# Kernel tuning notes

Hardware: AMD Instinct MI355X
Metric: run time of the kernel (lower is better)

The kernel has to match this reference:

```python
import jax, jax.numpy as jnp
import numpy as np
import math

FACTOR = 1

def setup_inputs() -> dict:
    key = jax.random.key(0)
    k1, k2, k3 = jax.random.split(key, 3)
    B, L, H, E = 32, 1024, 8, 64
    return {
        "queries": jax.random.normal(k1, (B, L, H, E), dtype=jnp.float32),
        "keys": jax.random.normal(k2, (B, L, H, E), dtype=jnp.float32),
        "values": jax.random.normal(k3, (B, L, H, E), dtype=jnp.float32),
        "attn_mask": 0,
    }


def reference(queries, keys, values, attn_mask):
    # queries/keys/values: [B, L, H, E] (S == L so no pad/truncate needed)
    B, L, H, E = queries.shape
    q = jnp.transpose(queries, (0, 2, 3, 1))  # [B,H,E,L]
    k = jnp.transpose(keys, (0, 2, 3, 1))
    v = jnp.transpose(values, (0, 2, 3, 1))   # [B,H,D,L]

    # FFT cross-correlation
    q_fft = jnp.fft.rfft(q, axis=-1)
    k_fft = jnp.fft.rfft(k, axis=-1)
    corr = jnp.fft.irfft(q_fft * jnp.conj(k_fft), n=L, axis=-1)  # [B,H,E,L]

    # top-k delay selection (global over batch, as in source)
    top_k = min(int(FACTOR * math.log(L)), L // 4, 32)  # static: 6
    mean_value = corr.mean(axis=(1, 2))                 # [B,L]
    weights, indices = jax.lax.top_k(mean_value.mean(axis=0), top_k)  # [k]
    tmp_corr = jax.nn.softmax(weights)                  # [k]

    # weighted circular-shift aggregation: roll(v, -indices[i]) summed with tmp_corr[i]
    pos = (jnp.arange(L)[None, :] + indices[:, None]) % L  # [k,L]
    patterns = v[:, :, :, pos]                              # [B,H,D,k,L]
    delays_agg = jnp.einsum('k,bhdkl->bhdl', tmp_corr, patterns)

    return jnp.transpose(delays_agg, (0, 3, 1, 2))  # [B,L,H,D]
```

## Files before the change

kernel.cpp:

```cpp
#include <hip/hip_runtime.h>
#include <math.h>

#define L_SEQ 1024
#define HE 512
#define NBATCH 32
#define TOPK 6
#define NZ 32

using bf16x8 = __attribute__((ext_vector_type(8))) short;
using f32x4  = __attribute__((ext_vector_type(4))) float;
using f32x2v = __attribute__((ext_vector_type(2))) float;
using bfx2v  = __attribute__((ext_vector_type(2))) __bf16;

__device__ __forceinline__ unsigned int bf2(float lo, float hi) {
  f32x2v f; f[0] = lo; f[1] = hi;
  bfx2v h = __builtin_convertvector(f, bfx2v);
  return *(unsigned int*)&h;
}

__global__ __launch_bounds__(512, 2) void gram_fused_kernel(
    const float* __restrict__ q, const float* __restrict__ k,
    float* __restrict__ partial)
{
  __shared__ char smem[71680];
  char* As = smem;
  char* Bs = smem + 32768;

  const int tid = threadIdx.x;
  const int l   = tid & 63;
  const int wid = tid >> 6;
  const int wrm = (wid >> 2) * 128;
  const int wcn = (wid & 3) * 64;
  const int s0  = blockIdx.x * 256;
  const int t0  = blockIdx.y * 256;
  const int z   = blockIdx.z;

  int swoff[4];
  size_t agoff[4], bgoff[4];
  #pragma unroll
  for (int it = 0; it < 4; ++it) {
    const int id  = (it << 9) | tid;
    const int row = id >> 3;
    const int c8  = id & 7;
    swoff[it] = ((row << 7) + (c8 << 4)) ^ ((row & 7) << 4);
    agoff[it] = (size_t)(s0 + row) * HE + c8 * 8;
    bgoff[it] = (size_t)(t0 + row) * HE + c8 * 8;
  }
  const size_t zbase = (size_t)z * L_SEQ * HE;

  f32x4 acc[8][4] = {};
  const int l15 = l & 15;
  const int blk = l >> 4;

  for (int t = 0; t < 8; ++t) {
    const size_t boff = zbase + t * 64;

    float4 ra0[4], ra1[4], rb0[4], rb1[4];
    #pragma unroll
    for (int it = 0; it < 4; ++it) {
      ra0[it] = *(const float4*)(q + boff + agoff[it]);
      ra1[it] = *(const float4*)(q + boff + agoff[it] + 4);
      rb0[it] = *(const float4*)(k + boff + bgoff[it]);
      rb1[it] = *(const float4*)(k + boff + bgoff[it] + 4);
    }

    __syncthreads();
    #pragma unroll
    for (int it = 0; it < 4; ++it) {
      uint4 pa, pb;
      pa.x = bf2(ra0[it].x, ra0[it].y); pa.y = bf2(ra0[it].z, ra0[it].w);
      pa.z = bf2(ra1[it].x, ra1[it].y); pa.w = bf2(ra1[it].z, ra1[it].w);
      pb.x = bf2(rb0[it].x, rb0[it].y); pb.y = bf2(rb0[it].z, rb0[it].w);
      pb.z = bf2(rb1[it].x, rb1[it].y); pb.w = bf2(rb1[it].z, rb1[it].w);
      *(uint4*)(As + swoff[it]) = pa;
      *(uint4*)(Bs + swoff[it]) = pb;
    }
    __syncthreads();

    #pragma unroll
    for (int kk = 0; kk < 2; ++kk) {
      bf16x8 bfr[4];
      #pragma unroll
      for (int n = 0; n < 4; ++n) {
        const int rowb = wcn + n * 16 + l15;
        const int offb = ((rowb << 7) + (kk << 6) + (blk << 4)) ^ ((rowb & 7) << 4);
        bfr[n] = *(const bf16x8*)(Bs + offb);
      }
      #pragma unroll
      for (int mh = 0; mh < 2; ++mh) {
        bf16x8 af[4];
        #pragma unroll
        for (int j = 0; j < 4; ++j) {
          const int rowa = wrm + (mh * 4 + j) * 16 + l15;
          const int offa = ((rowa << 7) + (kk << 6) + (blk << 4)) ^ ((rowa & 7) << 4);
          af[j] = *(const bf16x8*)(As + offa);
        }
        #pragma unroll
        for (int j = 0; j < 4; ++j)
          #pragma unroll
          for (int n = 0; n < 4; ++n)
            acc[mh * 4 + j][n] = __builtin_amdgcn_mfma_f32_16x16x32_bf16(
                af[j], bfr[n], acc[mh * 4 + j][n], 0, 0, 0);
      }
    }
  }

  float* Gs   = (float*)smem;
  float* bins = (float*)(smem + 67584);

  __syncthreads();
  for (int i = tid; i < 1024; i += 512) bins[i] = 0.f;

  #pragma unroll
  for (int cc = 0; cc < 4; ++cc) {
    __syncthreads();

    if ((wid >> 2) == (cc >> 1)) {
      #pragma unroll
      for (int mp = 0; mp < 4; ++mp) {
        const int m = (cc & 1) * 4 + mp;
        #pragma unroll
        for (int j = 0; j < 4; ++j) {
          const int ds = mp * 16 + blk * 4 + j;
          #pragma unroll
          for (int n = 0; n < 4; ++n)
            Gs[ds * 264 + wcn + n * 16 + l15] = acc[m][n][j];
        }
      }
    }
    __syncthreads();

    if (tid < 319) {
      const int o = tid - 255;
      float s = 0.f;
      #pragma unroll
      for (int i = 0; i < 64; ++i) {
        const int dt = i - o;
        const bool ok = (dt >= 0) && (dt < 256);
        const int dtc = ok ? dt : 0;
        const float v = Gs[i * 264 + dtc];
        s += ok ? v : 0.f;
      }
      const int tau = (s0 - t0 + 64 * cc + o + 4096) & (L_SEQ - 1);
      bins[tau] += s;
    }
  }
  __syncthreads();

  const int blin = blockIdx.x + 4 * blockIdx.y + 16 * blockIdx.z;
  for (int i = tid; i < 1024; i += 512)
    partial[(size_t)blin * 1024 + i] = bins[i];
}

__global__ __launch_bounds__(256) void reduce_kernel(
    const float* __restrict__ partial, float* __restrict__ c)
{
  const int tid = threadIdx.x;
  const int g16 = tid & 15;
  const int brow = tid >> 4;
  const int tau = blockIdx.x * 16 + g16;
  float s = 0.f;
  for (int it = 0; it < 32; ++it)
    s += partial[(size_t)(brow + (it << 4)) * 1024 + tau];
  __shared__ float sm[16][17];
  sm[brow][g16] = s;
  __syncthreads();
  if (tid < 16) {
    float t = 0.f;
    #pragma unroll
    for (int r = 0; r < 16; ++r) t += sm[r][tid];
    c[blockIdx.x * 16 + tid] = t * (1.0f / 16384.0f);
  }
}

__global__ __launch_bounds__(256) void topk_kernel(
    const float* __restrict__ c, int* __restrict__ idx_out,
    float* __restrict__ w_out)
{
  __shared__ float vals[L_SEQ];
  __shared__ float rv[256];
  __shared__ int ri[256];
  __shared__ float topv[TOPK];
  __shared__ int topi[TOPK];
  const int tid = threadIdx.x;
  for (int i = tid; i < L_SEQ; i += 256) vals[i] = c[i];
  __syncthreads();

  for (int kk = 0; kk < TOPK; ++kk) {
    float bv = -INFINITY;
    int bi = 1 << 30;
    for (int i = tid; i < L_SEQ; i += 256) {
      const float v = vals[i];
      if (v > bv || (v == bv && i < bi)) { bv = v; bi = i; }
    }
    rv[tid] = bv; ri[tid] = bi;
    __syncthreads();
    for (int off = 128; off > 0; off >>= 1) {
      if (tid < off) {
        const float v2 = rv[tid + off];
        const int i2 = ri[tid + off];
        if (v2 > rv[tid] || (v2 == rv[tid] && i2 < ri[tid])) {
          rv[tid] = v2; ri[tid] = i2;
        }
      }
      __syncthreads();
    }
    if (tid == 0) {
      topv[kk] = rv[0];
      topi[kk] = ri[0];
      vals[ri[0]] = -INFINITY;
    }
    __syncthreads();
  }

  if (tid == 0) {
    const float m = topv[0];
    float e[TOPK], sum = 0.f;
    for (int i = 0; i < TOPK; ++i) { e[i] = expf(topv[i] - m); sum += e[i]; }
    const float inv = 1.0f / sum;
    for (int i = 0; i < TOPK; ++i) { w_out[i] = e[i] * inv; idx_out[i] = topi[i]; }
  }
}

__global__ __launch_bounds__(256) void agg_kernel(
    const float* __restrict__ v, const int* __restrict__ idx,
    const float* __restrict__ w, float4* __restrict__ out)
{
  __shared__ int sidx[TOPK];
  __shared__ float sw[TOPK];
  if (threadIdx.x < TOPK) {
    sidx[threadIdx.x] = idx[threadIdx.x];
    sw[threadIdx.x] = w[threadIdx.x];
  }
  __syncthreads();

  const int i = blockIdx.x * 256 + threadIdx.x;
  const int he4 = i & 127;
  const int l = (i >> 7) & (L_SEQ - 1);
  const int b = i >> 17;
  const float4* vb = (const float4*)v + (size_t)b * (L_SEQ * 128);

  float4 acc = make_float4(0.f, 0.f, 0.f, 0.f);
  #pragma unroll
  for (int kk = 0; kk < TOPK; ++kk) {
    const int src = (l + sidx[kk]) & (L_SEQ - 1);
    const float4 vv = vb[(size_t)src * 128 + he4];
    const float wk = sw[kk];
    acc.x += wk * vv.x; acc.y += wk * vv.y;
    acc.z += wk * vv.z; acc.w += wk * vv.w;
  }
  out[i] = acc;
}

extern "C" void kernel_launch(void* const* d_in, const int* in_sizes, int n_in,
                              void* d_out, int out_size, void* d_ws, size_t ws_size,
                              hipStream_t stream) {
  const float* q = (const float*)d_in[0];
  const float* k = (const float*)d_in[1];
  const float* v = (const float*)d_in[2];

  float* out = (float*)d_out;
  float* partial = out;

  float* c = (float*)d_ws;
  int* idxp = (int*)((char*)d_ws + 4096);
  float* wp = (float*)((char*)d_ws + 4096 + 64);

  dim3 gGram(L_SEQ / 256, L_SEQ / 256, NZ);
  gram_fused_kernel<<<gGram, 512, 0, stream>>>(q, k, partial);
  reduce_kernel<<<64, 256, 0, stream>>>(partial, c);
  topk_kernel<<<1, 256, 0, stream>>>(c, idxp, wp);
  agg_kernel<<<(L_SEQ * NBATCH * 128) / 256, 256, 0, stream>>>(v, idxp, wp,
                                                               (float4*)out);
}
```

Measured before the change: 134.1 us.

## Double-buffer LDS tiles in gram kernel and fold two batches per block

The gram kernel now double-buffers the bf16 A/B tiles in 128KB of LDS. It prefetches the next K-slice from global memory into registers while the MFMAs for the current slice run, which removes one barrier per iteration. Each block now covers two batches (16 k-steps) instead of one, halving the z-grid and the partial-sum rows that the reduce kernel reads. It also raises MFMA wave priority with s_setprio and uses 32-bit offsets. The cost is that the larger LDS footprint cuts occupancy to one block per CU, and with 256 blocks fewer waves are available to hide latency.

```diff
diff --git a/kernel.cpp b/kernel.cpp
--- a/kernel.cpp
+++ b/kernel.cpp
@@ -5,7 +5,7 @@
 #define HE 512
 #define NBATCH 32
 #define TOPK 6
-#define NZ 32
+#define NZ 16
 
 using bf16x8 = __attribute__((ext_vector_type(8))) short;
 using f32x4  = __attribute__((ext_vector_type(4))) float;
@@ -22,9 +22,7 @@
     const float* __restrict__ q, const float* __restrict__ k,
     float* __restrict__ partial)
 {
-  __shared__ char smem[71680];
-  char* As = smem;
-  char* Bs = smem + 32768;
+  __shared__ char smem[131072];
 
   const int tid = threadIdx.x;
   const int l   = tid & 63;
@@ -36,26 +34,25 @@
   const int z   = blockIdx.z;
 
   int swoff[4];
-  size_t agoff[4], bgoff[4];
+  unsigned int agoff[4], bgoff[4];
   #pragma unroll
   for (int it = 0; it < 4; ++it) {
     const int id  = (it << 9) | tid;
     const int row = id >> 3;
     const int c8  = id & 7;
     swoff[it] = ((row << 7) + (c8 << 4)) ^ ((row & 7) << 4);
-    agoff[it] = (size_t)(s0 + row) * HE + c8 * 8;
-    bgoff[it] = (size_t)(t0 + row) * HE + c8 * 8;
-  }
-  const size_t zbase = (size_t)z * L_SEQ * HE;
+    agoff[it] = (unsigned int)(s0 + row) * HE + c8 * 8;
+    bgoff[it] = (unsigned int)(t0 + row) * HE + c8 * 8;
+  }
 
   f32x4 acc[8][4] = {};
   const int l15 = l & 15;
   const int blk = l >> 4;
 
-  for (int t = 0; t < 8; ++t) {
-    const size_t boff = zbase + t * 64;
-
-    float4 ra0[4], ra1[4], rb0[4], rb1[4];
+  float4 ra0[4], ra1[4], rb0[4], rb1[4];
+
+  {
+    const unsigned int boff = (unsigned int)(z * 2) * L_SEQ * HE;
     #pragma unroll
     for (int it = 0; it < 4; ++it) {
       ra0[it] = *(const float4*)(q + boff + agoff[it]);
@@ -63,8 +60,6 @@
       rb0[it] = *(const float4*)(k + boff + bgoff[it]);
       rb1[it] = *(const float4*)(k + boff + bgoff[it] + 4);
     }
-
-    __syncthreads();
     #pragma unroll
     for (int it = 0; it < 4; ++it) {
       uint4 pa, pb;
@@ -72,11 +67,28 @@
       pa.z = bf2(ra1[it].x, ra1[it].y); pa.w = bf2(ra1[it].z, ra1[it].w);
       pb.x = bf2(rb0[it].x, rb0[it].y); pb.y = bf2(rb0[it].z, rb0[it].w);
       pb.z = bf2(rb1[it].x, rb1[it].y); pb.w = bf2(rb1[it].z, rb1[it].w);
-      *(uint4*)(As + swoff[it]) = pa;
-      *(uint4*)(Bs + swoff[it]) = pb;
-    }
-    __syncthreads();
-
+      *(uint4*)(smem + swoff[it])         = pa;
+      *(uint4*)(smem + 32768 + swoff[it]) = pb;
+    }
+  }
+  __syncthreads();
+
+  for (int t = 0; t < 16; ++t) {
+    if (t < 15) {
+      const int tn = t + 1;
+      const unsigned int boff =
+          (unsigned int)(z * 2 + (tn >> 3)) * L_SEQ * HE + (tn & 7) * 64;
+      #pragma unroll
+      for (int it = 0; it < 4; ++it) {
+        ra0[it] = *(const float4*)(q + boff + agoff[it]);
+        ra1[it] = *(const float4*)(q + boff + agoff[it] + 4);
+        rb0[it] = *(const float4*)(k + boff + bgoff[it]);
+        rb1[it] = *(const float4*)(k + boff + bgoff[it] + 4);
+      }
+    }
+
+    const char* rbase = smem + ((t & 1) << 16);
+    __builtin_amdgcn_s_setprio(1);
     #pragma unroll
     for (int kk = 0; kk < 2; ++kk) {
       bf16x8 bfr[4];
@@ -84,7 +96,7 @@
       for (int n = 0; n < 4; ++n) {
         const int rowb = wcn + n * 16 + l15;
         const int offb = ((rowb << 7) + (kk << 6) + (blk << 4)) ^ ((rowb & 7) << 4);
-        bfr[n] = *(const bf16x8*)(Bs + offb);
+        bfr[n] = *(const bf16x8*)(rbase + 32768 + offb);
       }
       #pragma unroll
       for (int mh = 0; mh < 2; ++mh) {
@@ -93,7 +105,7 @@
         for (int j = 0; j < 4; ++j) {
           const int rowa = wrm + (mh * 4 + j) * 16 + l15;
           const int offa = ((rowa << 7) + (kk << 6) + (blk << 4)) ^ ((rowa & 7) << 4);
-          af[j] = *(const bf16x8*)(As + offa);
+          af[j] = *(const bf16x8*)(rbase + offa);
         }
         #pragma unroll
         for (int j = 0; j < 4; ++j)
@@ -103,12 +115,27 @@
                 af[j], bfr[n], acc[mh * 4 + j][n], 0, 0, 0);
       }
     }
+    __builtin_amdgcn_s_setprio(0);
+
+    if (t < 15) {
+      char* wbase = smem + (((t + 1) & 1) << 16);
+      #pragma unroll
+      for (int it = 0; it < 4; ++it) {
+        uint4 pa, pb;
+        pa.x = bf2(ra0[it].x, ra0[it].y); pa.y = bf2(ra0[it].z, ra0[it].w);
+        pa.z = bf2(ra1[it].x, ra1[it].y); pa.w = bf2(ra1[it].z, ra1[it].w);
+        pb.x = bf2(rb0[it].x, rb0[it].y); pb.y = bf2(rb0[it].z, rb0[it].w);
+        pb.z = bf2(rb1[it].x, rb1[it].y); pb.w = bf2(rb1[it].z, rb1[it].w);
+        *(uint4*)(wbase + swoff[it])         = pa;
+        *(uint4*)(wbase + 32768 + swoff[it]) = pb;
+      }
+    }
+    __syncthreads();
   }
 
   float* Gs   = (float*)smem;
   float* bins = (float*)(smem + 67584);
 
-  __syncthreads();
   for (int i = tid; i < 1024; i += 512) bins[i] = 0.f;
 
   #pragma unroll
@@ -160,7 +187,7 @@
   const int brow = tid >> 4;
   const int tau = blockIdx.x * 16 + g16;
   float s = 0.f;
-  for (int it = 0; it < 32; ++it)
+  for (int it = 0; it < 16; ++it)
     s += partial[(size_t)(brow + (it << 4)) * 1024 + tau];
   __shared__ float sm[16][17];
   sm[brow][g16] = s;
```

Measured after the change: 122.3 us. -8.8%, faster.

## Double-buffer Gram tiles via direct global-to-LDS loads with smaller tiles

Applied to the files above, without the earlier changes.

Restructures the Gram kernel to 128x128 output tiles with 256 threads, each block looping over 4 batches (NZ=8) along the K dimension. It uses global_load_lds to copy fp32 data straight into double-buffered LDS, prefetching the next step while computing the current one, and converts to bf16 after reading from LDS. The aim is to overlap memory with MFMA work and drop the register staging round trip. The cost is twice the LDS traffic for fp32 tiles and more work in the diagonal-binning epilogue per output element.

```diff
diff --git a/kernel.cpp b/kernel.cpp
--- a/kernel.cpp
+++ b/kernel.cpp
@@ -5,7 +5,8 @@
 #define HE 512
 #define NBATCH 32
 #define TOPK 6
-#define NZ 32
+#define NZ 8
+#define NT 64
 
 using bf16x8 = __attribute__((ext_vector_type(8))) short;
 using f32x4  = __attribute__((ext_vector_type(4))) float;
@@ -18,137 +19,146 @@
   return *(unsigned int*)&h;
 }
 
-__global__ __launch_bounds__(512, 2) void gram_fused_kernel(
+__device__ __forceinline__ bf16x8 pack8(float4 a, float4 b) {
+  unsigned int u[4] = {bf2(a.x, a.y), bf2(a.z, a.w), bf2(b.x, b.y), bf2(b.z, b.w)};
+  return *(bf16x8*)u;
+}
+
+__device__ __forceinline__ void gload_lds16(const float* g, char* l) {
+  __builtin_amdgcn_global_load_lds(
+      (const __attribute__((address_space(1))) void*)g,
+      (__attribute__((address_space(3))) void*)l, 16, 0, 0);
+}
+
+__global__ __launch_bounds__(256, 2) void gram_fused_kernel(
     const float* __restrict__ q, const float* __restrict__ k,
     float* __restrict__ partial)
 {
-  __shared__ char smem[71680];
-  char* As = smem;
-  char* Bs = smem + 32768;
+  __shared__ char smem[65536];
 
   const int tid = threadIdx.x;
   const int l   = tid & 63;
   const int wid = tid >> 6;
-  const int wrm = (wid >> 2) * 128;
-  const int wcn = (wid & 3) * 64;
-  const int s0  = blockIdx.x * 256;
-  const int t0  = blockIdx.y * 256;
+  const int wrm = (wid >> 1) * 64;
+  const int wcn = (wid & 1) * 64;
+  const int s0  = blockIdx.x * 128;
+  const int t0  = blockIdx.y * 128;
   const int z   = blockIdx.z;
 
-  int swoff[4];
-  size_t agoff[4], bgoff[4];
-  #pragma unroll
-  for (int it = 0; it < 4; ++it) {
-    const int id  = (it << 9) | tid;
-    const int row = id >> 3;
-    const int c8  = id & 7;
-    swoff[it] = ((row << 7) + (c8 << 4)) ^ ((row & 7) << 4);
-    agoff[it] = (size_t)(s0 + row) * HE + c8 * 8;
-    bgoff[it] = (size_t)(t0 + row) * HE + c8 * 8;
-  }
-  const size_t zbase = (size_t)z * L_SEQ * HE;
-
-  f32x4 acc[8][4] = {};
+  unsigned int aoff[4], boff[4];
+  int ldsoff[4];
+  #pragma unroll
+  for (int i = 0; i < 4; ++i) {
+    const int row = (wid * 4 + i) * 8 + (l >> 3);
+    const int hsrc = (l & 7) ^ (row & 7);
+    ldsoff[i] = (wid * 4 + i) * 1024;
+    aoff[i] = (unsigned int)(s0 + row) * HE + (hsrc << 2);
+    boff[i] = (unsigned int)(t0 + row) * HE + (hsrc << 2);
+  }
+
+  f32x4 acc[4][4] = {};
   const int l15 = l & 15;
   const int blk = l >> 4;
 
-  for (int t = 0; t < 8; ++t) {
-    const size_t boff = zbase + t * 64;
-
-    float4 ra0[4], ra1[4], rb0[4], rb1[4];
+  int ra0[4], ra1[4], rb0[4], rb1[4];
+  #pragma unroll
+  for (int f = 0; f < 4; ++f) {
+    const int rowa = wrm + f * 16 + l15;
+    ra0[f] = rowa * 128 + ((((blk << 1) | 0) ^ (rowa & 7)) << 4);
+    ra1[f] = rowa * 128 + ((((blk << 1) | 1) ^ (rowa & 7)) << 4);
+    const int rowb = wcn + f * 16 + l15;
+    rb0[f] = rowb * 128 + ((((blk << 1) | 0) ^ (rowb & 7)) << 4);
+    rb1[f] = rowb * 128 + ((((blk << 1) | 1) ^ (rowb & 7)) << 4);
+  }
+
+  #define KSTEP_BASE(t) \
+    ((unsigned int)(4 * z + ((t) >> 4)) * (L_SEQ * HE) + (((t) & 15) << 5))
+  #define STAGE(t, p) do {                                         \
+    const unsigned int ub = KSTEP_BASE(t);                         \
+    char* Ab_ = smem + ((p) << 15);                                \
+    char* Bb_ = Ab_ + 16384;                                       \
+    _Pragma("unroll")                                              \
+    for (int i_ = 0; i_ < 4; ++i_) {                               \
+      gload_lds16(q + ub + aoff[i_], Ab_ + ldsoff[i_]);            \
+      gload_lds16(k + ub + boff[i_], Bb_ + ldsoff[i_]);            \
+    }                                                              \
+  } while (0)
+
+  STAGE(0, 0);
+  __syncthreads();
+
+  for (int t = 0; t < NT; ++t) {
+    if (t + 1 < NT) STAGE(t + 1, (t + 1) & 1);
+
+    const char* Ab = smem + ((t & 1) << 15);
+    const char* Bb = Ab + 16384;
+
+    bf16x8 af[4], bfr[4];
     #pragma unroll
-    for (int it = 0; it < 4; ++it) {
-      ra0[it] = *(const float4*)(q + boff + agoff[it]);
-      ra1[it] = *(const float4*)(q + boff + agoff[it] + 4);
-      rb0[it] = *(const float4*)(k + boff + bgoff[it]);
-      rb1[it] = *(const float4*)(k + boff + bgoff[it] + 4);
-    }
-
-    __syncthreads();
+    for (int f = 0; f < 4; ++f) {
+      const float4 a0 = *(const float4*)(Ab + ra0[f]);
+      const float4 a1 = *(const float4*)(Ab + ra1[f]);
+      af[f] = pack8(a0, a1);
+      const float4 b0 = *(const float4*)(Bb + rb0[f]);
+      const float4 b1 = *(const float4*)(Bb + rb1[f]);
+      bfr[f] = pack8(b0, b1);
+    }
+
+    __builtin_amdgcn_s_setprio(1);
     #pragma unroll
-    for (int it = 0; it < 4; ++it) {
-      uint4 pa, pb;
-      pa.x = bf2(ra0[it].x, ra0[it].y); pa.y = bf2(ra0[it].z, ra0[it].w);
-      pa.z = bf2(ra1[it].x, ra1[it].y); pa.w = bf2(ra1[it].z, ra1[it].w);
-      pb.x = bf2(rb0[it].x, rb0[it].y); pb.y = bf2(rb0[it].z, rb0[it].w);
-      pb.z = bf2(rb1[it].x, rb1[it].y); pb.w = bf2(rb1[it].z, rb1[it].w);
-      *(uint4*)(As + swoff[it]) = pa;
-      *(uint4*)(Bs + swoff[it]) = pb;
-    }
-    __syncthreads();
-
-    #pragma unroll
-    for (int kk = 0; kk < 2; ++kk) {
-      bf16x8 bfr[4];
+    for (int m = 0; m < 4; ++m)
       #pragma unroll
-      for (int n = 0; n < 4; ++n) {
-        const int rowb = wcn + n * 16 + l15;
-        const int offb = ((rowb << 7) + (kk << 6) + (blk << 4)) ^ ((rowb & 7) << 4);
-        bfr[n] = *(const bf16x8*)(Bs + offb);
-      }
+      for (int n = 0; n < 4; ++n)
+        acc[m][n] = __builtin_amdgcn_mfma_f32_16x16x32_bf16(
+            af[m], bfr[n], acc[m][n], 0, 0, 0);
+    __builtin_amdgcn_s_setprio(0);
+
+    __syncthreads();
+  }
+
+  float* Gs   = (float*)smem;
+  float* bins = (float*)(smem + 16896);
+
+  for (int i = tid; i < 1024; i += 256) bins[i] = 0.f;
+
+  #pragma unroll
+  for (int cc = 0; cc < 4; ++cc) {
+    __syncthreads();
+
+    if ((wid >> 1) == (cc >> 1)) {
       #pragma unroll
-      for (int mh = 0; mh < 2; ++mh) {
-        bf16x8 af[4];
-        #pragma unroll
-        for (int j = 0; j < 4; ++j) {
-          const int rowa = wrm + (mh * 4 + j) * 16 + l15;
-          const int offa = ((rowa << 7) + (kk << 6) + (blk << 4)) ^ ((rowa & 7) << 4);
-          af[j] = *(const bf16x8*)(As + offa);
-        }
-        #pragma unroll
-        for (int j = 0; j < 4; ++j)
-          #pragma unroll
-          for (int n = 0; n < 4; ++n)
-            acc[mh * 4 + j][n] = __builtin_amdgcn_mfma_f32_16x16x32_bf16(
-                af[j], bfr[n], acc[mh * 4 + j][n], 0, 0, 0);
-      }
-    }
-  }
-
-  float* Gs   = (float*)smem;
-  float* bins = (float*)(smem + 67584);
-
-  __syncthreads();
-  for (int i = tid; i < 1024; i += 512) bins[i] = 0.f;
-
-  #pragma unroll
-  for (int cc = 0; cc < 4; ++cc) {
-    __syncthreads();
-
-    if ((wid >> 2) == (cc >> 1)) {
-      #pragma unroll
-      for (int mp = 0; mp < 4; ++mp) {
-        const int m = (cc & 1) * 4 + mp;
+      for (int mp = 0; mp < 2; ++mp) {
+        const int m = (cc & 1) * 2 + mp;
         #pragma unroll
         for (int j = 0; j < 4; ++j) {
           const int ds = mp * 16 + blk * 4 + j;
           #pragma unroll
           for (int n = 0; n < 4; ++n)
-            Gs[ds * 264 + wcn + n * 16 + l15] = acc[m][n][j];
+            Gs[ds * 132 + wcn + n * 16 + l15] = acc[m][n][j];
         }
       }
     }
     __syncthreads();
 
-    if (tid < 319) {
-      const int o = tid - 255;
+    if (tid < 159) {
+      const int o = tid - 127;
       float s = 0.f;
       #pragma unroll
-      for (int i = 0; i < 64; ++i) {
+      for (int i = 0; i < 32; ++i) {
         const int dt = i - o;
-        const bool ok = (dt >= 0) && (dt < 256);
+        const bool ok = (dt >= 0) && (dt < 128);
         const int dtc = ok ? dt : 0;
-        const float v = Gs[i * 264 + dtc];
+        const float v = Gs[i * 132 + dtc];
         s += ok ? v : 0.f;
       }
-      const int tau = (s0 - t0 + 64 * cc + o + 4096) & (L_SEQ - 1);
+      const int tau = (s0 - t0 + 32 * cc + o + 4096) & (L_SEQ - 1);
       bins[tau] += s;
     }
   }
   __syncthreads();
 
-  const int blin = blockIdx.x + 4 * blockIdx.y + 16 * blockIdx.z;
-  for (int i = tid; i < 1024; i += 512)
+  const int blin = blockIdx.x + 8 * blockIdx.y + 64 * blockIdx.z;
+  for (int i = tid; i < 1024; i += 256)
     partial[(size_t)blin * 1024 + i] = bins[i];
 }
 
@@ -266,8 +276,8 @@
   int* idxp = (int*)((char*)d_ws + 4096);
   float* wp = (float*)((char*)d_ws + 4096 + 64);
 
-  dim3 gGram(L_SEQ / 256, L_SEQ / 256, NZ);
-  gram_fused_kernel<<<gGram, 512, 0, stream>>>(q, k, partial);
+  dim3 gGram(L_SEQ / 128, L_SEQ / 128, NZ);
+  gram_fused_kernel<<<gGram, 256, 0, stream>>>(q, k, partial);
   reduce_kernel<<<64, 256, 0, stream>>>(partial, c);
   topk_kernel<<<1, 256, 0, stream>>>(c, idxp, wp);
   agg_kernel<<<(L_SEQ * NBATCH * 128) / 256, 256, 0, stream>>>(v, idxp, wp,
```

New measurement: 140.9 us. 1.05x slower.

## Double-buffer LDS in gram kernel, process two batches per block, swizzle block order

Applied to the files above, without the earlier changes.

The gram kernel now uses two LDS buffers so the global loads for the next K-step are issued before the MFMA phase on the current buffer, and each block covers two batches (16 K-steps), which halves the grid and the number of partial rows. Block IDs are remapped for locality, offsets are narrowed to 32-bit, and s_setprio raises priority during the MFMA phase. The aim is to hide global-load latency behind compute and cut launch and epilogue overhead. The cost is 128KB of LDS per block, which limits occupancy to one block per CU, and a grid of only 256 blocks.

```diff
diff --git a/kernel.cpp b/kernel.cpp
--- a/kernel.cpp
+++ b/kernel.cpp
@@ -5,7 +5,8 @@
 #define HE 512
 #define NBATCH 32
 #define TOPK 6
-#define NZ 32
+#define NZ 16
+#define NT 16
 
 using bf16x8 = __attribute__((ext_vector_type(8))) short;
 using f32x4  = __attribute__((ext_vector_type(4))) float;
@@ -22,88 +23,112 @@
     const float* __restrict__ q, const float* __restrict__ k,
     float* __restrict__ partial)
 {
-  __shared__ char smem[71680];
-  char* As = smem;
-  char* Bs = smem + 32768;
+  __shared__ char smem[131072];
+
+  const int bid = blockIdx.x + 4 * blockIdx.y + 16 * blockIdx.z;
+  const int swz = (bid & 7) * 32 + (bid >> 3);
+  const int bx = swz & 3, by = (swz >> 2) & 3, bz = swz >> 4;
 
   const int tid = threadIdx.x;
   const int l   = tid & 63;
   const int wid = tid >> 6;
   const int wrm = (wid >> 2) * 128;
   const int wcn = (wid & 3) * 64;
-  const int s0  = blockIdx.x * 256;
-  const int t0  = blockIdx.y * 256;
-  const int z   = blockIdx.z;
+  const int s0  = bx * 256;
+  const int t0  = by * 256;
+  const int z   = bz;
 
   int swoff[4];
-  size_t agoff[4], bgoff[4];
+  unsigned int agoff[4], bgoff[4];
   #pragma unroll
   for (int it = 0; it < 4; ++it) {
     const int id  = (it << 9) | tid;
     const int row = id >> 3;
     const int c8  = id & 7;
     swoff[it] = ((row << 7) + (c8 << 4)) ^ ((row & 7) << 4);
-    agoff[it] = (size_t)(s0 + row) * HE + c8 * 8;
-    bgoff[it] = (size_t)(t0 + row) * HE + c8 * 8;
-  }
-  const size_t zbase = (size_t)z * L_SEQ * HE;
+    agoff[it] = (unsigned int)(s0 + row) * HE + c8 * 8;
+    bgoff[it] = (unsigned int)(t0 + row) * HE + c8 * 8;
+  }
 
   f32x4 acc[8][4] = {};
   const int l15 = l & 15;
   const int blk = l >> 4;
 
-  for (int t = 0; t < 8; ++t) {
-    const size_t boff = zbase + t * 64;
-
-    float4 ra0[4], ra1[4], rb0[4], rb1[4];
-    #pragma unroll
-    for (int it = 0; it < 4; ++it) {
-      ra0[it] = *(const float4*)(q + boff + agoff[it]);
-      ra1[it] = *(const float4*)(q + boff + agoff[it] + 4);
-      rb0[it] = *(const float4*)(k + boff + bgoff[it]);
-      rb1[it] = *(const float4*)(k + boff + bgoff[it] + 4);
-    }
-
-    __syncthreads();
-    #pragma unroll
-    for (int it = 0; it < 4; ++it) {
-      uint4 pa, pb;
-      pa.x = bf2(ra0[it].x, ra0[it].y); pa.y = bf2(ra0[it].z, ra0[it].w);
-      pa.z = bf2(ra1[it].x, ra1[it].y); pa.w = bf2(ra1[it].z, ra1[it].w);
-      pb.x = bf2(rb0[it].x, rb0[it].y); pb.y = bf2(rb0[it].z, rb0[it].w);
-      pb.z = bf2(rb1[it].x, rb1[it].y); pb.w = bf2(rb1[it].z, rb1[it].w);
-      *(uint4*)(As + swoff[it]) = pa;
-      *(uint4*)(Bs + swoff[it]) = pb;
-    }
-    __syncthreads();
-
-    #pragma unroll
-    for (int kk = 0; kk < 2; ++kk) {
-      bf16x8 bfr[4];
-      #pragma unroll
-      for (int n = 0; n < 4; ++n) {
-        const int rowb = wcn + n * 16 + l15;
-        const int offb = ((rowb << 7) + (kk << 6) + (blk << 4)) ^ ((rowb & 7) << 4);
-        bfr[n] = *(const bf16x8*)(Bs + offb);
-      }
-      #pragma unroll
-      for (int mh = 0; mh < 2; ++mh) {
-        bf16x8 af[4];
-        #pragma unroll
-        for (int j = 0; j < 4; ++j) {
-          const int rowa = wrm + (mh * 4 + j) * 16 + l15;
-          const int offa = ((rowa << 7) + (kk << 6) + (blk << 4)) ^ ((rowa & 7) << 4);
-          af[j] = *(const bf16x8*)(As + offa);
-        }
-        #pragma unroll
-        for (int j = 0; j < 4; ++j)
-          #pragma unroll
-          for (int n = 0; n < 4; ++n)
-            acc[mh * 4 + j][n] = __builtin_amdgcn_mfma_f32_16x16x32_bf16(
-                af[j], bfr[n], acc[mh * 4 + j][n], 0, 0, 0);
-      }
-    }
-  }
+  float4 ra0[4], ra1[4], rb0[4], rb1[4];
+
+  #define LOADSTEP(t) do {                                                  \
+    const unsigned int boff =                                               \
+        (unsigned int)(z * 2 + ((t) >> 3)) * (L_SEQ * HE) + ((t) & 7) * 64; \
+    _Pragma("unroll")                                                       \
+    for (int it_ = 0; it_ < 4; ++it_) {                                     \
+      ra0[it_] = *(const float4*)(q + boff + agoff[it_]);                   \
+      ra1[it_] = *(const float4*)(q + boff + agoff[it_] + 4);               \
+      rb0[it_] = *(const float4*)(k + boff + bgoff[it_]);                   \
+      rb1[it_] = *(const float4*)(k + boff + bgoff[it_] + 4);               \
+    }                                                                       \
+  } while (0)
+
+  #define PACKWRITE(p) do {                                                 \
+    char* wbase_ = smem + ((p) << 16);                                      \
+    _Pragma("unroll")                                                       \
+    for (int it_ = 0; it_ < 4; ++it_) {                                     \
+      uint4 pa_, pb_;                                                       \
+      pa_.x = bf2(ra0[it_].x, ra0[it_].y); pa_.y = bf2(ra0[it_].z, ra0[it_].w); \
+      pa_.z = bf2(ra1[it_].x, ra1[it_].y); pa_.w = bf2(ra1[it_].z, ra1[it_].w); \
+      pb_.x = bf2(rb0[it_].x, rb0[it_].y); pb_.y = bf2(rb0[it_].z, rb0[it_].w); \
+      pb_.z = bf2(rb1[it_].x, rb1[it_].y); pb_.w = bf2(rb1[it_].z, rb1[it_].w); \
+      *(uint4*)(wbase_ + swoff[it_])         = pa_;                         \
+      *(uint4*)(wbase_ + 32768 + swoff[it_]) = pb_;                         \
+    }                                                                       \
+  } while (0)
+
+  #define MFMAPHASE(t) do {                                                 \
+    const char* rbase = smem + (((t) & 1) << 16);                           \
+    __builtin_amdgcn_s_setprio(1);                                          \
+    _Pragma("unroll")                                                       \
+    for (int kk = 0; kk < 2; ++kk) {                                        \
+      bf16x8 bfr[4];                                                        \
+      _Pragma("unroll")                                                     \
+      for (int n = 0; n < 4; ++n) {                                         \
+        const int rowb = wcn + n * 16 + l15;                                \
+        const int offb =                                                    \
+            ((rowb << 7) + (kk << 6) + (blk << 4)) ^ ((rowb & 7) << 4);     \
+        bfr[n] = *(const bf16x8*)(rbase + 32768 + offb);                    \
+      }                                                                     \
+      _Pragma("unroll")                                                     \
+      for (int mh = 0; mh < 2; ++mh) {                                      \
+        bf16x8 af[4];                                                       \
+        _Pragma("unroll")                                                   \
+        for (int j = 0; j < 4; ++j) {                                       \
+          const int rowa = wrm + (mh * 4 + j) * 16 + l15;                   \
+          const int offa =                                                  \
+              ((rowa << 7) + (kk << 6) + (blk << 4)) ^ ((rowa & 7) << 4);   \
+          af[j] = *(const bf16x8*)(rbase + offa);                           \
+        }                                                                   \
+        _Pragma("unroll")                                                   \
+        for (int j = 0; j < 4; ++j)                                         \
+          _Pragma("unroll")                                                 \
+          for (int n = 0; n < 4; ++n)                                       \
+            acc[mh * 4 + j][n] = __builtin_amdgcn_mfma_f32_16x16x32_bf16(   \
+                af[j], bfr[n], acc[mh * 4 + j][n], 0, 0, 0);                \
+      }                                                                     \
+    }                                                                       \
+    __builtin_amdgcn_s_setprio(0);                                          \
+  } while (0)
+
+  LOADSTEP(0);
+  PACKWRITE(0);
+  __syncthreads();
+
+  for (int t = 0; t < NT - 1; ++t) {
+    LOADSTEP(t + 1);
+    __builtin_amdgcn_sched_barrier(0);
+    MFMAPHASE(t);
+    __builtin_amdgcn_sched_barrier(0);
+    PACKWRITE((t + 1) & 1);
+    __syncthreads();
+  }
+  MFMAPHASE(NT - 1);
 
   float* Gs   = (float*)smem;
   float* bins = (float*)(smem + 67584);
@@ -147,7 +172,7 @@
   }
   __syncthreads();
 
-  const int blin = blockIdx.x + 4 * blockIdx.y + 16 * blockIdx.z;
+  const int blin = bx + 4 * by + 16 * bz;
   for (int i = tid; i < 1024; i += 512)
     partial[(size_t)blin * 1024 + i] = bins[i];
 }
@@ -160,7 +185,7 @@
   const int brow = tid >> 4;
   const int tau = blockIdx.x * 16 + g16;
   float s = 0.f;
-  for (int it = 0; it < 32; ++it)
+  for (int it = 0; it < 16; ++it)
     s += partial[(size_t)(brow + (it << 4)) * 1024 + tau];
   __shared__ float sm[16][17];
   sm[brow][g16] = s;
```

Measured after the change: 110.7 us. 1.21x faster.
